# Kernel optimization log

Hardware: AMD Instinct MI355X
Metric: run time of the kernel (lower is better)

## Reference

```python
import jax, jax.numpy as jnp
import numpy as np

B, S, D, H = 4, 2048, 2048, 16
HD = D // H  # 128


def _rope(t, cos, sin):
    # t: [B, S, H, HD]; cos/sin: [S, HD//2]
    tr = t.reshape(t.shape[:-1] + (HD // 2, 2))
    t1, t2 = tr[..., 0], tr[..., 1]
    c = cos[None, :, None, :]
    s = sin[None, :, None, :]
    o1 = t1 * c - t2 * s
    o2 = t1 * s + t2 * c
    return jnp.stack([o1, o2], axis=-1).reshape(t.shape)


def setup_inputs() -> dict:
    key = jax.random.key(0)
    ks = jax.random.split(key, 9)
    init_std = HD ** -0.5
    pos = jnp.arange(S, dtype=jnp.float32)[:, None]
    inv = 1.0 / (10000.0 ** (jnp.arange(0, HD, 2, dtype=jnp.float32) / HD))
    ang = pos * inv[None, :]
    return {
        "x": jax.random.normal(ks[0], (B, S, D), jnp.float32),
        "query": jax.random.normal(ks[1], (B, S, D), jnp.float32),
        "value": jax.random.normal(ks[2], (B, S, D), jnp.float32),
        "freqs_cos": jnp.cos(ang),
        "freqs_sin": jnp.sin(ang),
        "key_w": jax.random.normal(ks[3], (D, D), jnp.float32) * init_std,
        "key_b": jnp.zeros((D,), jnp.float32),
        "proj_w": jax.random.normal(ks[4], (D, D), jnp.float32) * init_std,
        "proj_b": jnp.zeros((D,), jnp.float32),
    }


def reference(x, query, value, freqs_cos, freqs_sin, key_w, key_b, proj_w, proj_b):
    # key projection applied to x; query/value arrive pre-projected
    k = (jnp.einsum("bsd,ed->bse", x, key_w) + key_b).reshape(B, S, H, HD)
    q = query.reshape(B, S, H, HD)
    v = value.reshape(B, S, H, HD)
    q = _rope(q, freqs_cos, freqs_sin)
    k = _rope(k, freqs_cos, freqs_sin)
    scale = 1.0 / np.sqrt(HD)
    scores = jnp.einsum("bqhd,bkhd->bhqk", q, k) * scale  # [B,H,S,S]
    causal = jnp.tril(jnp.ones((S, S), bool))
    scores = jnp.where(causal[None, None], scores, jnp.finfo(scores.dtype).min)
    probs = jax.nn.softmax(scores, axis=-1)
    out = jnp.einsum("bhqk,bkhd->bqhd", probs, v).reshape(B, S, D)
    return jnp.einsum("bsd,ed->bse", out, proj_w) + proj_b
```

## Files before the change

kernel.cpp:

```cpp
#include <hip/hip_runtime.h>
#include <hip/hip_bf16.h>
#include <stdint.h>

#define BB 4
#define SS 2048
#define DD 2048
#define HH 16
#define HD 128
#define MTOT (BB*SS)

typedef __attribute__((ext_vector_type(8))) short short8;
typedef __attribute__((ext_vector_type(4))) float f32x4;

__device__ __forceinline__ unsigned short f2bf(float f) {
    union { float f; unsigned int u; } v; v.f = f;
    unsigned int u = v.u;
    return (unsigned short)((u + 0x7FFFu + ((u >> 16) & 1u)) >> 16);
}

__global__ __launch_bounds__(256) void convert_kernel(
    const float* __restrict__ src, unsigned short* __restrict__ dst, int n4) {
    int i = blockIdx.x * 256 + threadIdx.x;
    if (i >= n4) return;
    float4 v = ((const float4*)src)[i];
    unsigned int lo = (unsigned int)f2bf(v.x) | ((unsigned int)f2bf(v.y) << 16);
    unsigned int hi = (unsigned int)f2bf(v.z) | ((unsigned int)f2bf(v.w) << 16);
    ((uint2*)dst)[i] = make_uint2(lo, hi);
}

__global__ __launch_bounds__(256) void rope_q_kernel(
    const float* __restrict__ q, const float* __restrict__ fc,
    const float* __restrict__ fs, unsigned short* __restrict__ dst) {
    int idx = blockIdx.x * 256 + threadIdx.x;
    int row   = idx >> 10;
    int s     = row & (SS - 1);
    int p     = idx & 63;
    float2 t = ((const float2*)q)[idx];
    float c = fc[s*64 + p], sn = fs[s*64 + p];
    float o1 = t.x*c - t.y*sn;
    float o2 = t.x*sn + t.y*c;
    ((unsigned int*)dst)[idx] = (unsigned int)f2bf(o1) | ((unsigned int)f2bf(o2) << 16);
}

__global__ __launch_bounds__(256) void transpose_v_kernel(
    const float* __restrict__ v, unsigned short* __restrict__ vt) {
    __shared__ unsigned short tile[64][72];
    int bh = blockIdx.z;
    int s0 = blockIdx.x * 64, d0 = blockIdx.y * 64;
    int t = threadIdx.x;
    #pragma unroll
    for (int it = 0; it < 4; ++it) {
        int i  = it*16 + (t >> 4);
        int j4 = t & 15;
        float4 f = *(const float4*)(v +
            (((size_t)((bh >> 4)*SS + s0 + i)*HH + (bh & 15))*HD + d0 + j4*4));
        unsigned int lo = (unsigned int)f2bf(f.x) | ((unsigned int)f2bf(f.y) << 16);
        unsigned int hi = (unsigned int)f2bf(f.z) | ((unsigned int)f2bf(f.w) << 16);
        *(uint2*)&tile[i][j4*4] = make_uint2(lo, hi);
    }
    __syncthreads();
    unsigned int* vt32 = (unsigned int*)vt;
    #pragma unroll
    for (int it = 0; it < 8; ++it) {
        int task = it*256 + t;
        int sp = task & 31;
        int d  = task >> 5;
        unsigned int lo = tile[2*sp][d], hi = tile[2*sp + 1][d];
        vt32[((size_t)bh*HD + d0 + d)*(SS/2) + (s0 >> 1) + sp] = lo | (hi << 16);
    }
}

template<int MODE>
__global__ __launch_bounds__(256, 2) void gemm_kernel(
    const unsigned short* __restrict__ A, const unsigned short* __restrict__ W,
    const float* __restrict__ bias, const float* __restrict__ fc,
    const float* __restrict__ fs, void* __restrict__ out)
{
    __shared__ unsigned short As[128*32];
    __shared__ unsigned short Bs[128*32];
    const int K = DD;
    int m0 = blockIdx.y * 128, n0 = blockIdx.x * 128;
    int t = threadIdx.x, lane = t & 63, w = t >> 6;
    int wm = w >> 1, wn = w & 1;
    int l15 = lane & 15, quad = lane >> 4;

    f32x4 acc[4][4] = {};

    for (int k0 = 0; k0 < K; k0 += 32) {
        __syncthreads();
        #pragma unroll
        for (int i = 0; i < 2; ++i) {
            int ci  = i*256 + t;
            int row = ci >> 2;
            int ce  = (ci & 3) * 8;
            const unsigned short* ga = A + (size_t)(m0 + row) * K + k0 + ce;
            const unsigned short* gb = W + (size_t)(n0 + row) * K + k0 + ce;
            unsigned short* la = As + (size_t)(i*256 + w*64) * 8;
            unsigned short* lb = Bs + (size_t)(i*256 + w*64) * 8;
            __builtin_amdgcn_global_load_lds(
                (__attribute__((address_space(1))) void*)(uintptr_t)ga,
                (__attribute__((address_space(3))) void*)la, 16, 0, 0);
            __builtin_amdgcn_global_load_lds(
                (__attribute__((address_space(1))) void*)(uintptr_t)gb,
                (__attribute__((address_space(3))) void*)lb, 16, 0, 0);
        }
        __syncthreads();

        short8 af[4], bw[4];
        #pragma unroll
        for (int i = 0; i < 4; ++i) {
            af[i] = *(const short8*)(As + (size_t)(wm*64 + i*16 + l15)*32 + quad*8);
            bw[i] = *(const short8*)(Bs + (size_t)(wn*64 + i*16 + l15)*32 + quad*8);
        }
        #pragma unroll
        for (int i = 0; i < 4; ++i)
            #pragma unroll
            for (int j = 0; j < 4; ++j)
                acc[i][j] = __builtin_amdgcn_mfma_f32_16x16x32_bf16(
                    af[i], bw[j], acc[i][j], 0, 0, 0);
    }

    #pragma unroll
    for (int i = 0; i < 4; ++i) {
        #pragma unroll
        for (int j = 0; j < 4; ++j) {
            int col = n0 + wn*64 + j*16 + l15;
            float bv = bias[col];
            #pragma unroll
            for (int r = 0; r < 4; ++r) {
                int row = m0 + wm*64 + i*16 + quad*4 + r;
                float v = acc[i][j][r] + bv;
                if (MODE == 0) {
                    int s = row & (SS - 1);
                    int p = (col & 127) >> 1;
                    float other = __shfl_xor(v, 1);
                    float c = fc[s*64 + p], sn = fs[s*64 + p];
                    float res = (col & 1) ? (other*sn + v*c) : (v*c - other*sn);
                    ((unsigned short*)out)[(size_t)row*DD + col] = f2bf(res);
                } else {
                    ((float*)out)[(size_t)row*DD + col] = v;
                }
            }
        }
    }
}

__global__ __launch_bounds__(256, 3) void attn_kernel(
    const unsigned short* __restrict__ Q, const unsigned short* __restrict__ Kr,
    const unsigned short* __restrict__ Vt, unsigned short* __restrict__ O)
{
    constexpr int PSTR = 72;
    __shared__ unsigned short Ks[64*128];
    __shared__ unsigned short VTs[128*64];
    __shared__ unsigned short Ps[64*PSTR];

    int bh = blockIdx.y;
    int b = bh >> 4, h = bh & 15;
    size_t base  = (size_t)b*SS*DD + (size_t)h*HD;
    size_t vbase = (size_t)bh*HD*SS;

    int t = threadIdx.x, lane = t & 63, w = t >> 6;
    int l15 = lane & 15, quad = lane >> 4;
    int pair = blockIdx.x;
    int l7 = l15 & 7;

    const float scl2 = 0.08838834764831845f * 1.44269504088896f;

    for (int ph = 0; ph < 2; ++ph) {
        int qt = ph ? (31 - pair) : pair;
        int q0 = qt * 64;

        short8 aq[4];
        #pragma unroll
        for (int kk = 0; kk < 4; ++kk)
            aq[kk] = *(const short8*)(Q + base +
                (size_t)(q0 + w*16 + l15)*DD + kk*32 + quad*8);

        float m_i[4], l_i[4];
        #pragma unroll
        for (int r = 0; r < 4; ++r) { m_i[r] = -1e30f; l_i[r] = 0.f; }
        f32x4 o_acc[8] = {};

        for (int jt = 0; jt <= qt; ++jt) {
            int j0 = jt * 64;

            __syncthreads();
            #pragma unroll
            for (int i = 0; i < 4; ++i) {
                int ci  = i*256 + t;
                int row = ci >> 4;
                int cc  = ci & 15;
                int gch = cc ^ (row & 7);
                const unsigned short* ga =
                    Kr + base + (size_t)(j0 + row)*DD + gch*8;
                unsigned short* la = Ks + (size_t)(i*256 + w*64) * 8;
                __builtin_amdgcn_global_load_lds(
                    (__attribute__((address_space(1))) void*)(uintptr_t)ga,
                    (__attribute__((address_space(3))) void*)la, 16, 0, 0);
            }
            #pragma unroll
            for (int i = 0; i < 4; ++i) {
                int ci  = i*256 + t;
                int d   = ci >> 3;
                int cc  = ci & 7;
                int gch = cc ^ (d & 7);
                const unsigned short* ga =
                    Vt + vbase + (size_t)d*SS + j0 + gch*8;
                unsigned short* la = VTs + (size_t)(i*256 + w*64) * 8;
                __builtin_amdgcn_global_load_lds(
                    (__attribute__((address_space(1))) void*)(uintptr_t)ga,
                    (__attribute__((address_space(3))) void*)la, 16, 0, 0);
            }
            __syncthreads();

            f32x4 sacc[4];
            #pragma unroll
            for (int c = 0; c < 4; ++c) {
                sacc[c] = (f32x4){0.f, 0.f, 0.f, 0.f};
                #pragma unroll
                for (int kk = 0; kk < 4; ++kk) {
                    short8 bk = *(const short8*)(Ks +
                        (size_t)(c*16 + l15)*128 + ((kk*4 + quad) ^ l7)*8);
                    sacc[c] = __builtin_amdgcn_mfma_f32_16x16x32_bf16(aq[kk], bk, sacc[c], 0,0,0);
                }
            }

            bool diag = (jt == qt);
            float p[4][4], mt[4];
            #pragma unroll
            for (int r = 0; r < 4; ++r) mt[r] = -1e30f;
            #pragma unroll
            for (int c = 0; c < 4; ++c)
                #pragma unroll
                for (int r = 0; r < 4; ++r) {
                    float v = sacc[c][r] * scl2;
                    if (diag) {
                        int cg = c*16 + l15;
                        int rg = w*16 + quad*4 + r;
                        if (cg > rg) v = -1e30f;
                    }
                    p[c][r] = v;
                    mt[r] = fmaxf(mt[r], v);
                }
            #pragma unroll
            for (int r = 0; r < 4; ++r) {
                float m = mt[r];
                m = fmaxf(m, __shfl_xor(m, 1));
                m = fmaxf(m, __shfl_xor(m, 2));
                m = fmaxf(m, __shfl_xor(m, 4));
                m = fmaxf(m, __shfl_xor(m, 8));
                float mnew = fmaxf(m_i[r], m);
                mt[r] = exp2f(m_i[r] - mnew);
                m_i[r] = mnew;
            }
            float rs[4] = {0.f, 0.f, 0.f, 0.f};
            #pragma unroll
            for (int c = 0; c < 4; ++c)
                #pragma unroll
                for (int r = 0; r < 4; ++r) {
                    float e = exp2f(p[c][r] - m_i[r]);
                    p[c][r] = e;
                    rs[r] += e;
                }
            #pragma unroll
            for (int r = 0; r < 4; ++r) {
                float s = rs[r];
                s += __shfl_xor(s, 1);
                s += __shfl_xor(s, 2);
                s += __shfl_xor(s, 4);
                s += __shfl_xor(s, 8);
                l_i[r] = l_i[r]*mt[r] + s;
            }
            #pragma unroll
            for (int f = 0; f < 8; ++f)
                #pragma unroll
                for (int r = 0; r < 4; ++r)
                    o_acc[f][r] *= mt[r];

            #pragma unroll
            for (int c = 0; c < 4; ++c)
                #pragma unroll
                for (int r = 0; r < 4; ++r)
                    Ps[(size_t)(w*16 + quad*4 + r)*PSTR + c*16 + l15] = f2bf(p[c][r]);

            #pragma unroll
            for (int kk2 = 0; kk2 < 2; ++kk2) {
                short8 ap = *(const short8*)(Ps + (size_t)(w*16 + l15)*PSTR + kk2*32 + quad*8);
                #pragma unroll
                for (int f = 0; f < 8; ++f) {
                    short8 bv = *(const short8*)(VTs +
                        (size_t)(f*16 + l15)*64 + ((kk2*4 + quad) ^ l7)*8);
                    o_acc[f] = __builtin_amdgcn_mfma_f32_16x16x32_bf16(ap, bv, o_acc[f], 0,0,0);
                }
            }
        }

        #pragma unroll
        for (int f = 0; f < 8; ++f) {
            #pragma unroll
            for (int r = 0; r < 4; ++r) {
                int srow = q0 + w*16 + quad*4 + r;
                int d = f*16 + l15;
                O[base + (size_t)srow*DD + d] = f2bf(o_acc[f][r] / l_i[r]);
            }
        }
    }
}

extern "C" void kernel_launch(void* const* d_in, const int* in_sizes, int n_in,
                              void* d_out, int out_size, void* d_ws, size_t ws_size,
                              hipStream_t stream) {
    const float* x      = (const float*)d_in[0];
    const float* query  = (const float*)d_in[1];
    const float* value  = (const float*)d_in[2];
    const float* fc     = (const float*)d_in[3];
    const float* fs     = (const float*)d_in[4];
    const float* key_w  = (const float*)d_in[5];
    const float* key_b  = (const float*)d_in[6];
    const float* proj_w = (const float*)d_in[7];
    const float* proj_b = (const float*)d_in[8];

    const int ND  = BB*SS*DD;
    const int NW  = DD*DD;
    unsigned short* xb  = (unsigned short*)d_ws;
    unsigned short* kwb = xb  + ND;
    unsigned short* pwb = kwb + NW;
    unsigned short* qr  = pwb + NW;
    unsigned short* vt  = qr  + ND;
    unsigned short* kr  = vt  + ND;
    unsigned short* ao  = xb;

    convert_kernel<<<ND/4/256, 256, 0, stream>>>(x, xb, ND/4);
    convert_kernel<<<NW/4/256, 256, 0, stream>>>(key_w, kwb, NW/4);
    convert_kernel<<<NW/4/256, 256, 0, stream>>>(proj_w, pwb, NW/4);
    rope_q_kernel<<<ND/2/256, 256, 0, stream>>>(query, fc, fs, qr);
    transpose_v_kernel<<<dim3(SS/64, HD/64, BB*HH), 256, 0, stream>>>(value, vt);

    dim3 gg(DD/128, MTOT/128);
    gemm_kernel<0><<<gg, 256, 0, stream>>>(xb, kwb, key_b, fc, fs, (void*)kr);
    attn_kernel<<<dim3(16, BB*HH), 256, 0, stream>>>(qr, kr, vt, ao);
    gemm_kernel<1><<<gg, 256, 0, stream>>>(ao, pwb, proj_b, nullptr, nullptr, d_out);
}
```

Baseline: 653.1 us.

## Enlarge attention query tiles, add lazy rescaling, and swizzle block order

The attention kernel now uses 512 threads covering 128 query rows per block. Each K/V tile is loaded once and shared by twice as many rows, and waves whose rows are fully masked skip the compute. Online-softmax rescaling now runs only when the running max grows by more than a threshold, and P is written to shared memory straight from the exp loop with cheaper round-up bf16 conversion. Block indices in both the GEMM and attention kernels are remapped to improve L2 locality. The trade-offs are larger blocks that may lower occupancy, idle waves in causal tiles, and slightly changed rounding of P.

```diff
diff --git a/kernel.cpp b/kernel.cpp
--- a/kernel.cpp
+++ b/kernel.cpp
@@ -16,6 +16,10 @@
     union { float f; unsigned int u; } v; v.f = f;
     unsigned int u = v.u;
     return (unsigned short)((u + 0x7FFFu + ((u >> 16) & 1u)) >> 16);
+}
+__device__ __forceinline__ unsigned short f2bf_ru(float f) {
+    union { float f; unsigned int u; } v; v.f = f;
+    return (unsigned short)((v.u + 0x8000u) >> 16);
 }
 
 __global__ __launch_bounds__(256) void convert_kernel(
@@ -79,7 +83,9 @@
     __shared__ unsigned short As[128*32];
     __shared__ unsigned short Bs[128*32];
     const int K = DD;
-    int m0 = blockIdx.y * 128, n0 = blockIdx.x * 128;
+    int L   = blockIdx.y * 16 + blockIdx.x;
+    int swz = (L & 7) * 128 + (L >> 3);
+    int m0 = (swz >> 4) * 128, n0 = (swz & 15) * 128;
     int t = threadIdx.x, lane = t & 63, w = t >> 6;
     int wm = w >> 1, wn = w & 1;
     int l15 = lane & 15, quad = lane >> 4;
@@ -145,73 +151,80 @@
     }
 }
 
-__global__ __launch_bounds__(256, 3) void attn_kernel(
+__global__ __launch_bounds__(512, 4) void attn_kernel(
     const unsigned short* __restrict__ Q, const unsigned short* __restrict__ Kr,
     const unsigned short* __restrict__ Vt, unsigned short* __restrict__ O)
 {
     constexpr int PSTR = 72;
     __shared__ unsigned short Ks[64*128];
     __shared__ unsigned short VTs[128*64];
-    __shared__ unsigned short Ps[64*PSTR];
-
-    int bh = blockIdx.y;
+    __shared__ unsigned short Ps[128*PSTR];
+
+    int L   = blockIdx.y * 8 + blockIdx.x;
+    int swz = (L & 7) * 64 + (L >> 3);
+    int bh   = swz >> 3;
+    int pair = swz & 7;
+
     int b = bh >> 4, h = bh & 15;
     size_t base  = (size_t)b*SS*DD + (size_t)h*HD;
     size_t vbase = (size_t)bh*HD*SS;
 
     int t = threadIdx.x, lane = t & 63, w = t >> 6;
     int l15 = lane & 15, quad = lane >> 4;
-    int pair = blockIdx.x;
     int l7 = l15 & 7;
 
     const float scl2 = 0.08838834764831845f * 1.44269504088896f;
 
     for (int ph = 0; ph < 2; ++ph) {
-        int qt = ph ? (31 - pair) : pair;
-        int q0 = qt * 64;
+        int qt = ph ? (15 - pair) : pair;
+        int q0 = qt * 128;
+        int rw = q0 + w*16;
 
         short8 aq[4];
         #pragma unroll
         for (int kk = 0; kk < 4; ++kk)
             aq[kk] = *(const short8*)(Q + base +
-                (size_t)(q0 + w*16 + l15)*DD + kk*32 + quad*8);
+                (size_t)(rw + l15)*DD + kk*32 + quad*8);
 
         float m_i[4], l_i[4];
         #pragma unroll
         for (int r = 0; r < 4; ++r) { m_i[r] = -1e30f; l_i[r] = 0.f; }
         f32x4 o_acc[8] = {};
 
-        for (int jt = 0; jt <= qt; ++jt) {
+        int jmax = 2*qt + 1;
+        for (int jt = 0; jt <= jmax; ++jt) {
             int j0 = jt * 64;
 
             __syncthreads();
             #pragma unroll
-            for (int i = 0; i < 4; ++i) {
-                int ci  = i*256 + t;
+            for (int i = 0; i < 2; ++i) {
+                int ci  = i*512 + t;
                 int row = ci >> 4;
                 int cc  = ci & 15;
                 int gch = cc ^ (row & 7);
                 const unsigned short* ga =
                     Kr + base + (size_t)(j0 + row)*DD + gch*8;
-                unsigned short* la = Ks + (size_t)(i*256 + w*64) * 8;
+                unsigned short* la = Ks + (size_t)(i*512 + w*64) * 8;
                 __builtin_amdgcn_global_load_lds(
                     (__attribute__((address_space(1))) void*)(uintptr_t)ga,
                     (__attribute__((address_space(3))) void*)la, 16, 0, 0);
             }
             #pragma unroll
-            for (int i = 0; i < 4; ++i) {
-                int ci  = i*256 + t;
+            for (int i = 0; i < 2; ++i) {
+                int ci  = i*512 + t;
                 int d   = ci >> 3;
                 int cc  = ci & 7;
                 int gch = cc ^ (d & 7);
                 const unsigned short* ga =
                     Vt + vbase + (size_t)d*SS + j0 + gch*8;
-                unsigned short* la = VTs + (size_t)(i*256 + w*64) * 8;
+                unsigned short* la = VTs + (size_t)(i*512 + w*64) * 8;
                 __builtin_amdgcn_global_load_lds(
                     (__attribute__((address_space(1))) void*)(uintptr_t)ga,
                     (__attribute__((address_space(3))) void*)la, 16, 0, 0);
             }
             __syncthreads();
+
+            if (j0 > rw + 15) continue;
 
             f32x4 sacc[4];
             #pragma unroll
@@ -225,42 +238,59 @@
                 }
             }
 
-            bool diag = (jt == qt);
-            float p[4][4], mt[4];
-            #pragma unroll
-            for (int r = 0; r < 4; ++r) mt[r] = -1e30f;
+            bool diag = (j0 + 63 > rw);
+            float p[4][4], mt4[4];
+            #pragma unroll
+            for (int r = 0; r < 4; ++r) mt4[r] = -1e30f;
             #pragma unroll
             for (int c = 0; c < 4; ++c)
                 #pragma unroll
                 for (int r = 0; r < 4; ++r) {
                     float v = sacc[c][r] * scl2;
                     if (diag) {
-                        int cg = c*16 + l15;
-                        int rg = w*16 + quad*4 + r;
+                        int cg = j0 + c*16 + l15;
+                        int rg = rw + quad*4 + r;
                         if (cg > rg) v = -1e30f;
                     }
                     p[c][r] = v;
-                    mt[r] = fmaxf(mt[r], v);
-                }
+                    mt4[r] = fmaxf(mt4[r], v);
+                }
+
+            bool grow = false;
             #pragma unroll
             for (int r = 0; r < 4; ++r) {
-                float m = mt[r];
+                float m = mt4[r];
                 m = fmaxf(m, __shfl_xor(m, 1));
                 m = fmaxf(m, __shfl_xor(m, 2));
                 m = fmaxf(m, __shfl_xor(m, 4));
                 m = fmaxf(m, __shfl_xor(m, 8));
-                float mnew = fmaxf(m_i[r], m);
-                mt[r] = exp2f(m_i[r] - mnew);
-                m_i[r] = mnew;
-            }
+                mt4[r] = m;
+                grow = grow || (m > m_i[r] + 8.0f);
+            }
+            if (__any(grow)) {
+                #pragma unroll
+                for (int r = 0; r < 4; ++r) {
+                    float mn = fmaxf(m_i[r], mt4[r]);
+                    float a  = exp2f(m_i[r] - mn);
+                    m_i[r] = mn;
+                    l_i[r] *= a;
+                    mt4[r] = a;
+                }
+                #pragma unroll
+                for (int f = 0; f < 8; ++f)
+                    #pragma unroll
+                    for (int r = 0; r < 4; ++r)
+                        o_acc[f][r] *= mt4[r];
+            }
+
             float rs[4] = {0.f, 0.f, 0.f, 0.f};
             #pragma unroll
             for (int c = 0; c < 4; ++c)
                 #pragma unroll
                 for (int r = 0; r < 4; ++r) {
                     float e = exp2f(p[c][r] - m_i[r]);
-                    p[c][r] = e;
                     rs[r] += e;
+                    Ps[(size_t)(w*16 + quad*4 + r)*PSTR + c*16 + l15] = f2bf_ru(e);
                 }
             #pragma unroll
             for (int r = 0; r < 4; ++r) {
@@ -269,19 +299,8 @@
                 s += __shfl_xor(s, 2);
                 s += __shfl_xor(s, 4);
                 s += __shfl_xor(s, 8);
-                l_i[r] = l_i[r]*mt[r] + s;
-            }
-            #pragma unroll
-            for (int f = 0; f < 8; ++f)
-                #pragma unroll
-                for (int r = 0; r < 4; ++r)
-                    o_acc[f][r] *= mt[r];
-
-            #pragma unroll
-            for (int c = 0; c < 4; ++c)
-                #pragma unroll
-                for (int r = 0; r < 4; ++r)
-                    Ps[(size_t)(w*16 + quad*4 + r)*PSTR + c*16 + l15] = f2bf(p[c][r]);
+                l_i[r] += s;
+            }
 
             #pragma unroll
             for (int kk2 = 0; kk2 < 2; ++kk2) {
@@ -299,7 +318,7 @@
         for (int f = 0; f < 8; ++f) {
             #pragma unroll
             for (int r = 0; r < 4; ++r) {
-                int srow = q0 + w*16 + quad*4 + r;
+                int srow = rw + quad*4 + r;
                 int d = f*16 + l15;
                 O[base + (size_t)srow*DD + d] = f2bf(o_acc[f][r] / l_i[r]);
             }
@@ -338,6 +357,6 @@
 
     dim3 gg(DD/128, MTOT/128);
     gemm_kernel<0><<<gg, 256, 0, stream>>>(xb, kwb, key_b, fc, fs, (void*)kr);
-    attn_kernel<<<dim3(16, BB*HH), 256, 0, stream>>>(qr, kr, vt, ao);
+    attn_kernel<<<dim3(8, BB*HH), 512, 0, stream>>>(qr, kr, vt, ao);
     gemm_kernel<1><<<gg, 256, 0, stream>>>(ao, pwb, proj_b, nullptr, nullptr, d_out);
 }
```

After: 577.8 us. -11.5%, faster.
